# Performance work log

Hardware: AMD Instinct MI355X
Metric: run time of the kernel (lower is better)

## Reference

```python
import jax, jax.numpy as jnp
import numpy as np

N, M, E, D = 100000, 20000, 1600000, 128


def setup_inputs() -> dict:
    key = jax.random.key(0)
    ks = jax.random.split(key, 14)
    s = 1.0 / np.sqrt(D)
    inp = {
        "x": jax.random.normal(ks[0], (N, D), jnp.float32),
        "in_src": jax.random.randint(ks[1], (E,), 0, N),
        "in_dst": jax.random.randint(ks[2], (E,), 0, M),
        "has_src": jax.random.randint(ks[3], (E,), 0, M),
        "has_dst": jax.random.randint(ks[4], (E,), 0, N),
        "W1": jax.random.normal(ks[5], (D, D), jnp.float32) * s,
        "b1": jnp.zeros((D,), jnp.float32),
        "an1": jax.random.normal(ks[6], (D, 1), jnp.float32) * s,
        "ae1": jax.random.normal(ks[7], (D, 1), jnp.float32) * s,
        "W2": jax.random.normal(ks[8], (D, D), jnp.float32) * s,
        "b2": jnp.zeros((D,), jnp.float32),
        "an2": jax.random.normal(ks[9], (D, 1), jnp.float32) * s,
        "ae2": jax.random.normal(ks[10], (D, 1), jnp.float32) * s,
    }
    return inp


def _hgat_layer(x, W, b, an, ae, in_src, in_dst, has_src, has_dst, activate):
    h = x @ W + b                       # [N, D] fc transform
    n_attn = h @ an                     # [N, 1] node attn scores
    # node -> hyperedge ('in' edges). h_e is unset at this point (local_scope),
    # so the hyperedge bias term is zero; e = attn[src].
    e = n_attn[in_src]                  # [E, 1]
    # source uses F.softmax(e, dim=0): GLOBAL softmax over all edges
    attn = jax.nn.softmax(e, axis=0)    # [E, 1]
    h_e = jax.ops.segment_sum(attn * h[in_src], in_dst, num_segments=M)  # [M, D]
    e_attn = h_e @ ae                   # [M, 1] hyperedge attn scores
    # hyperedge -> node ('has' edges): bias is node attn score at dst
    e2 = e_attn[has_src] + n_attn[has_dst]  # [E, 1]
    attn2 = jax.nn.softmax(e2, axis=0)      # global softmax over all edges
    h_n = jax.ops.segment_sum(attn2 * h_e[has_src], has_dst, num_segments=N)  # [N, D]
    return jax.nn.relu(h_n) if activate else h_n


def reference(x, in_src, in_dst, has_src, has_dst,
              W1, b1, an1, ae1, W2, b2, an2, ae2):
    # layer 1 (activation=relu), layer 2 (no activation); dropout in eval mode
    h = _hgat_layer(x, W1, b1, an1, ae1, in_src, in_dst, has_src, has_dst, True)
    h = _hgat_layer(h, W2, b2, an2, ae2, in_src, in_dst, has_src, has_dst, False)
    return h
```

## Files before the change

kernel.cpp:

```cpp
#include <hip/hip_runtime.h>
#include <hip/hip_bf16.h>
#include <math.h>


typedef unsigned int u32;
typedef unsigned short u16;
typedef u16 u16x8 __attribute__((ext_vector_type(8)));
typedef short bf16x8 __attribute__((ext_vector_type(8)));
typedef float f32x4 __attribute__((ext_vector_type(4)));

#define NCONST 100000
#define MCONST 20000
#define ECONST 1600000
#define HCH2 32768
#define HBC 32
#define NCH_N 4

#define PBLK 256
#define PT 6250
#define SHB_IN 6
#define NBK_IN 313
#define SRCB_IN 17
#define SHB_HAS 8
#define NBK_HAS 391
#define SRCB_HAS 15

__device__ __forceinline__ u16 f2bf(float f) {
  u32 u = __float_as_uint(f);
  u += 0x7FFFu + ((u >> 16) & 1u);
  return (u16)(u >> 16);
}
__device__ __forceinline__ float bf2f(u16 b) {
  return __uint_as_float(((u32)b) << 16);
}

__global__ __launch_bounds__(256) void k_hpart2(const int* __restrict__ in_dst,
                                                const int* __restrict__ has_dst,
                                                int* __restrict__ partial) {
  __shared__ int hc[HCH2];
  int y = blockIdx.y;
  const int* __restrict__ arr = (y == 0) ? in_dst : has_dst;
  int lo = (y == 0) ? 0 : (y - 1) * HCH2;
  for (int i = threadIdx.x; i < HCH2; i += 256) hc[i] = 0;
  __syncthreads();
  int stride = gridDim.x * 256;
  int n4 = ECONST >> 2;
  const int4* a4 = (const int4*)arr;
  for (int i = blockIdx.x * 256 + threadIdx.x; i < n4; i += stride) {
    int4 v = a4[i];
    u32 a = (u32)(v.x - lo), b = (u32)(v.y - lo), c = (u32)(v.z - lo), d = (u32)(v.w - lo);
    if (a < HCH2) atomicAdd(&hc[a], 1);
    if (b < HCH2) atomicAdd(&hc[b], 1);
    if (c < HCH2) atomicAdd(&hc[c], 1);
    if (d < HCH2) atomicAdd(&hc[d], 1);
  }
  __syncthreads();
  int* out = partial + ((size_t)y * HBC + blockIdx.x) * HCH2;
  for (int i = threadIdx.x; i < HCH2; i += 256) out[i] = hc[i];
}

__global__ void k_scan1d(const int* __restrict__ partial, int nM, int nN,
                         int* __restrict__ off_in, int* __restrict__ off_has,
                         int* __restrict__ bsum) {
  __shared__ int sd[256];
  int y = blockIdx.y;
  int n = y ? nN : nM;
  int yoff = y;
  int* off = y ? off_has : off_in;
  int* bs = bsum + y * 128;
  int t = threadIdx.x;
  int base = blockIdx.x * 1024 + t * 4;
  int v[4];
#pragma unroll
  for (int k = 0; k < 4; ++k) {
    int j = base + k;
    int s = 0;
    if (j < n) {
      int chunk = j >> 15;
      int jl = j & (HCH2 - 1);
      const int* p = partial + ((size_t)(yoff + chunk) * HBC) * HCH2 + jl;
#pragma unroll
      for (int b = 0; b < HBC; ++b) s += p[(size_t)b * HCH2];
    }
    v[k] = s;
  }
  v[1] += v[0]; v[2] += v[1]; v[3] += v[2];
  int tot = v[3];
  sd[t] = tot;
  __syncthreads();
  for (int o = 1; o < 256; o <<= 1) {
    int x = (t >= o) ? sd[t - o] : 0;
    __syncthreads();
    sd[t] += x;
    __syncthreads();
  }
  int excl = sd[t] - tot;
#pragma unroll
  for (int k = 0; k < 4; ++k)
    if (base + k < n) off[base + k + 1] = v[k] + excl;
  if (t == 255) bs[blockIdx.x] = sd[255];
}

__global__ void k_scan2d(int* __restrict__ bsum, int nbM, int nbN) {
  __shared__ int sd[256];
  int* bs = bsum + blockIdx.x * 128;
  int nb = blockIdx.x ? nbN : nbM;
  int t = threadIdx.x;
  int v = (t < nb) ? bs[t] : 0;
  sd[t] = v;
  __syncthreads();
  for (int o = 1; o < 256; o <<= 1) {
    int x = (t >= o) ? sd[t - o] : 0;
    __syncthreads();
    sd[t] += x;
    __syncthreads();
  }
  if (t < nb) bs[t] = sd[t] - v;
}

__global__ void k_scan3d(int* __restrict__ off_in, int* __restrict__ off_has,
                         const int* __restrict__ bsum, int nM, int nN) {
  int y = blockIdx.y;
  int* off = y ? off_has : off_in;
  const int* bs = bsum + y * 128;
  int n = y ? nN : nM;
  int i = blockIdx.x * blockDim.x + threadIdx.x;
  int st = gridDim.x * blockDim.x;
  if (blockIdx.x == 0 && threadIdx.x == 0) off[0] = 0;
  for (; i < n; i += st) off[i + 1] += bs[i >> 10];
}

__global__ __launch_bounds__(256) void k_coarse(const int* __restrict__ in_dst,
                                                const int* __restrict__ has_dst,
                                                int* __restrict__ bb_in,
                                                int* __restrict__ bb_has) {
  __shared__ int h1[NBK_IN];
  __shared__ int h2[NBK_HAS];
  for (int i = threadIdx.x; i < NBK_IN; i += 256) h1[i] = 0;
  for (int i = threadIdx.x; i < NBK_HAS; i += 256) h2[i] = 0;
  __syncthreads();
  int c0 = blockIdx.x * PT, c1 = min(c0 + PT, ECONST);
  for (int i = c0 + threadIdx.x; i < c1; i += 256) {
    atomicAdd(&h1[in_dst[i] >> SHB_IN], 1);
    atomicAdd(&h2[has_dst[i] >> SHB_HAS], 1);
  }
  __syncthreads();
  int* o1 = bb_in + (size_t)blockIdx.x * NBK_IN;
  for (int i = threadIdx.x; i < NBK_IN; i += 256) o1[i] = h1[i];
  int* o2 = bb_has + (size_t)blockIdx.x * NBK_HAS;
  for (int i = threadIdx.x; i < NBK_HAS; i += 256) o2[i] = h2[i];
}

__global__ __launch_bounds__(256) void k_colscan(int* __restrict__ bb, int nbuk,
                                                 const int* __restrict__ off, int shb,
                                                 int segs) {
  __shared__ int sd[256];
  int b = blockIdx.x;
  int t = threadIdx.x;
  int v = bb[(size_t)t * nbuk + b];
  sd[t] = v;
  __syncthreads();
  for (int o = 1; o < 256; o <<= 1) {
    int x = (t >= o) ? sd[t - o] : 0;
    __syncthreads();
    sd[t] += x;
    __syncthreads();
  }
  bb[(size_t)t * nbuk + b] = sd[t] - v + off[min(b << shb, segs)];
}

template <int NBUK, int SHB, int SRCB>
__global__ __launch_bounds__(256) void k_stage(const int* __restrict__ dst,
                                               const int* __restrict__ srcv,
                                               const int* __restrict__ bb,
                                               int* __restrict__ ebuf) {
  __shared__ int hist[NBUK];
  __shared__ int loff[NBUK];
  __shared__ int gbase[NBUK];
  __shared__ int stage[PT];
  __shared__ int sd[256];
  int t = threadIdx.x;
  for (int i = t; i < NBUK; i += 256) hist[i] = 0;
  __syncthreads();
  int c0 = blockIdx.x * PT, c1 = min(c0 + PT, ECONST);
  for (int i = c0 + t; i < c1; i += 256) atomicAdd(&hist[dst[i] >> SHB], 1);
  __syncthreads();
  {
    int v0 = (2 * t < NBUK) ? hist[2 * t] : 0;
    int v1 = (2 * t + 1 < NBUK) ? hist[2 * t + 1] : 0;
    sd[t] = v0 + v1;
    __syncthreads();
    for (int o = 1; o < 256; o <<= 1) {
      int x = (t >= o) ? sd[t - o] : 0;
      __syncthreads();
      sd[t] += x;
      __syncthreads();
    }
    int excl = sd[t] - (v0 + v1);
    if (2 * t < NBUK) loff[2 * t] = excl;
    if (2 * t + 1 < NBUK) loff[2 * t + 1] = excl + v0;
  }
  __syncthreads();
  for (int i = t; i < NBUK; i += 256) {
    gbase[i] = bb[(size_t)blockIdx.x * NBUK + i];
    hist[i] = loff[i];
  }
  __syncthreads();
  for (int i = c0 + t; i < c1; i += 256) {
    int d = dst[i], s = srcv[i];
    int b = d >> SHB;
    int r = atomicAdd(&hist[b], 1);
    stage[r] = (b << 23) | ((d & ((1 << SHB) - 1)) << SRCB) | s;
  }
  __syncthreads();
  int tot = c1 - c0;
  for (int i = t; i < tot; i += 256) {
    int v = stage[i];
    int b = ((u32)v) >> 23;
    ebuf[gbase[b] + (i - loff[b])] = v & ((1 << 23) - 1);
  }
}

template <int SHB, int SRCB>
__global__ __launch_bounds__(256) void k_place(const int* __restrict__ off, int segs,
                                               const int* __restrict__ ebuf,
                                               int* __restrict__ csrc) {
  const int NSEG = 1 << SHB;
  __shared__ int cur[NSEG];
  int seg0 = blockIdx.x << SHB;
  if (seg0 >= segs) return;
  int segN = min(seg0 + NSEG, segs);
  for (int i = threadIdx.x; i < segN - seg0; i += 256) cur[i] = off[seg0 + i];
  __syncthreads();
  int start = off[seg0], end = off[segN];
  for (int i = start + threadIdx.x; i < end; i += 256) {
    int v = ebuf[i];
    int dloc = ((u32)v) >> SRCB;
    int pos = atomicAdd(&cur[dloc], 1);
    csrc[pos] = v & ((1 << SRCB) - 1);
  }
}

template <typename IT>
__global__ __launch_bounds__(256, 2) void k_fc(
    const IT* __restrict__ x, const float* __restrict__ W,
    const float* __restrict__ bias, const float* __restrict__ an,
    u16* __restrict__ h, float* __restrict__ na, int nrows) {
  __shared__ __align__(16) u16 sWT[128 * 136];
  int tid = threadIdx.x;
  int lane = tid & 63, w = tid >> 6;
  int cl = lane & 15, qg = lane >> 4;

  for (int i = tid * 4; i < 16384; i += 1024) {
    float4 v = *(const float4*)(W + i);
    int k = i >> 7, j = i & 127;
    sWT[(j + 0) * 136 + k] = f2bf(v.x);
    sWT[(j + 1) * 136 + k] = f2bf(v.y);
    sWT[(j + 2) * 136 + k] = f2bf(v.z);
    sWT[(j + 3) * 136 + k] = f2bf(v.w);
  }

  float anv[8], bv[8];
#pragma unroll
  for (int t = 0; t < 8; ++t) {
    anv[t] = an[t * 16 + cl];
    bv[t] = bias[t * 16 + cl];
  }

  int rbase = blockIdx.x * 128 + w * 32;
  bf16x8 afr[2][4];
#pragma unroll
  for (int g = 0; g < 2; ++g) {
    int r = rbase + g * 16 + cl;
    int rc = min(r, nrows - 1);
    const IT* xp = x + (size_t)rc * 128 + qg * 8;
#pragma unroll
    for (int s = 0; s < 4; ++s) {
      if constexpr (sizeof(IT) == 4) {
        float4 u0 = *(const float4*)(xp + s * 32);
        float4 u1 = *(const float4*)(xp + s * 32 + 4);
        bf16x8 a;
        a[0] = (short)f2bf(u0.x); a[1] = (short)f2bf(u0.y);
        a[2] = (short)f2bf(u0.z); a[3] = (short)f2bf(u0.w);
        a[4] = (short)f2bf(u1.x); a[5] = (short)f2bf(u1.y);
        a[6] = (short)f2bf(u1.z); a[7] = (short)f2bf(u1.w);
        afr[g][s] = a;
      } else {
        afr[g][s] = *(const bf16x8*)(xp + s * 32);
      }
    }
  }
  __syncthreads();

  f32x4 acc[2][8];
#pragma unroll
  for (int g = 0; g < 2; ++g)
#pragma unroll
    for (int t = 0; t < 8; ++t) {
      acc[g][t][0] = 0.f; acc[g][t][1] = 0.f; acc[g][t][2] = 0.f; acc[g][t][3] = 0.f;
    }

#pragma unroll
  for (int t = 0; t < 8; ++t) {
    bf16x8 bfrg[4];
    const u16* bp = sWT + (t * 16 + cl) * 136 + qg * 8;
#pragma unroll
    for (int s = 0; s < 4; ++s) bfrg[s] = *(const bf16x8*)(bp + s * 32);
#pragma unroll
    for (int s = 0; s < 4; ++s) {
#pragma unroll
      for (int g = 0; g < 2; ++g)
        acc[g][t] = __builtin_amdgcn_mfma_f32_16x16x32_bf16(afr[g][s], bfrg[s], acc[g][t],
                                                            0, 0, 0);
    }
  }

  float pa[2][4];
#pragma unroll
  for (int g = 0; g < 2; ++g)
#pragma unroll
    for (int reg = 0; reg < 4; ++reg) pa[g][reg] = 0.f;
#pragma unroll
  for (int g = 0; g < 2; ++g)
#pragma unroll
    for (int t = 0; t < 8; ++t)
#pragma unroll
      for (int reg = 0; reg < 4; ++reg)
        pa[g][reg] = fmaf(acc[g][t][reg] + bv[t], anv[t], pa[g][reg]);
#pragma unroll
  for (int g = 0; g < 2; ++g)
#pragma unroll
    for (int reg = 0; reg < 4; ++reg) {
      float v = pa[g][reg];
      v += __shfl_xor(v, 1, 64);
      v += __shfl_xor(v, 2, 64);
      v += __shfl_xor(v, 4, 64);
      v += __shfl_xor(v, 8, 64);
      pa[g][reg] = v;
    }
  if (cl == 0) {
#pragma unroll
    for (int g = 0; g < 2; ++g)
#pragma unroll
      for (int reg = 0; reg < 4; ++reg) {
        int r = rbase + g * 16 + qg * 4 + reg;
        if (r < nrows) na[r] = pa[g][reg];
      }
  }

  __syncthreads();
  u16* st = sWT + w * 32 * 136;
#pragma unroll
  for (int g = 0; g < 2; ++g)
#pragma unroll
    for (int t = 0; t < 8; ++t)
#pragma unroll
      for (int reg = 0; reg < 4; ++reg)
        st[(g * 16 + qg * 4 + reg) * 136 + t * 16 + cl] = f2bf(acc[g][t][reg] + bv[t]);
#pragma unroll
  for (int it = 0; it < 8; ++it) {
    int idx = it * 64 + lane;
    int row = idx >> 4, c = idx & 15;
    u16x8 v = *(const u16x8*)(st + row * 136 + c * 8);
    int r = rbase + row;
    if (r < nrows) *(u16x8*)(h + (size_t)r * 128 + c * 8) = v;
  }
}

__device__ __forceinline__ void merge_write(float m, float s, float2* __restrict__ pairs) {
  for (int o = 1; o < 64; o <<= 1) {
    float om = __shfl_xor(m, o, 64), os = __shfl_xor(s, o, 64);
    float nm = fmaxf(m, om);
    s = s * __expf(m - nm) + os * __expf(om - nm);
    m = nm;
  }
  __shared__ float sm[4], ss[4];
  int t = threadIdx.x;
  if ((t & 63) == 0) { sm[t >> 6] = m; ss[t >> 6] = s; }
  __syncthreads();
  if (t == 0) {
    for (int k = 1; k < 4; ++k) {
      float nm = fmaxf(m, sm[k]);
      s = s * __expf(m - nm) + ss[k] * __expf(sm[k] - nm);
      m = nm;
    }
    pairs[blockIdx.x] = make_float2(m, s);
  }
}

__global__ void k_sm1e(const float* __restrict__ na, const int* __restrict__ src, int n,
                       float2* __restrict__ pairs) {
  float m = -1e30f, s = 0.f;
  int i = blockIdx.x * blockDim.x + threadIdx.x;
  int st = gridDim.x * blockDim.x;
  for (; i < n; i += st) {
    float xv = na[src[i]];
    if (xv > m) { s *= __expf(m - xv); m = xv; }
    s += __expf(xv - m);
  }
  merge_write(m, s, pairs);
}

__global__ void k_sm2(const float* __restrict__ ea, const float* __restrict__ na,
                      const int* __restrict__ hs, const int* __restrict__ hd, int n,
                      float2* __restrict__ pairs) {
  float m = -1e30f, s = 0.f;
  int i = blockIdx.x * blockDim.x + threadIdx.x;
  int st = gridDim.x * blockDim.x;
  for (; i < n; i += st) {
    float xv = ea[hs[i]] + na[hd[i]];
    if (xv > m) { s *= __expf(m - xv); m = xv; }
    s += __expf(xv - m);
  }
  merge_write(m, s, pairs);
}

__global__ void k_smfin(const float2* __restrict__ pairs, int nb, float* __restrict__ out) {
  int t = threadIdx.x;
  float m = -1e30f, s = 0.f;
  for (int i = t; i < nb; i += 256) {
    float2 pr = pairs[i];
    float nm = fmaxf(m, pr.x);
    s = s * __expf(m - nm) + pr.y * __expf(pr.x - nm);
    m = nm;
  }
  for (int o = 1; o < 64; o <<= 1) {
    float om = __shfl_xor(m, o, 64), os = __shfl_xor(s, o, 64);
    float nm = fmaxf(m, om);
    s = s * __expf(m - nm) + os * __expf(om - nm);
    m = nm;
  }
  __shared__ float sm[4], ss[4];
  if ((t & 63) == 0) { sm[t >> 6] = m; ss[t >> 6] = s; }
  __syncthreads();
  if (t == 0) {
    for (int k = 1; k < 4; ++k) {
      float nm = fmaxf(m, sm[k]);
      s = s * __expf(m - nm) + ss[k] * __expf(sm[k] - nm);
      m = nm;
    }
    out[0] = m;
    out[1] = s;
  }
}

__global__ __launch_bounds__(256) void k_segA(
    const u16* __restrict__ h, const float* __restrict__ na,
    const float* __restrict__ scal, const int* __restrict__ csrc,
    const int* __restrict__ off, const float* __restrict__ ae, u16* __restrict__ he,
    float* __restrict__ ea, int m_count) {
  int wid = (blockIdx.x << 2) + (threadIdx.x >> 6);
  if (wid >= m_count) return;
  float mx = scal[0];
  float iz = 1.0f / scal[1];
  int lane = threadIdx.x & 63;
  int sub = lane >> 4, cl = lane & 15;
  int s = off[wid], t = off[wid + 1];
  float ax[8];
#pragma unroll
  for (int j = 0; j < 8; ++j) ax[j] = 0.f;
  for (int i = s + sub; i < t; i += 4) {
    int sr = csrc[i];
    float ww = __expf(na[sr] - mx) * iz;
    u16x8 v = *(const u16x8*)(h + (size_t)sr * 128 + cl * 8);
#pragma unroll
    for (int j = 0; j < 8; ++j) ax[j] = fmaf(ww, bf2f(v[j]), ax[j]);
  }
#pragma unroll
  for (int j = 0; j < 8; ++j) {
    ax[j] += __shfl_xor(ax[j], 16, 64);
    ax[j] += __shfl_xor(ax[j], 32, 64);
  }
  float4 a0 = *(const float4*)(ae + cl * 8);
  float4 a1 = *(const float4*)(ae + cl * 8 + 4);
  float pa = ax[0] * a0.x + ax[1] * a0.y + ax[2] * a0.z + ax[3] * a0.w +
             ax[4] * a1.x + ax[5] * a1.y + ax[6] * a1.z + ax[7] * a1.w;
  pa += __shfl_xor(pa, 1, 64);
  pa += __shfl_xor(pa, 2, 64);
  pa += __shfl_xor(pa, 4, 64);
  pa += __shfl_xor(pa, 8, 64);
  if (sub == 0) {
    u16x8 o;
#pragma unroll
    for (int j = 0; j < 8; ++j) o[j] = f2bf(ax[j]);
    *(u16x8*)(he + (size_t)wid * 128 + cl * 8) = o;
    if (cl == 0) ea[wid] = pa;
  }
}

template <int L1>
__global__ __launch_bounds__(256) void k_segB(
    const u16* __restrict__ he, const float* __restrict__ ea,
    const float* __restrict__ na, const float* __restrict__ scal,
    const int* __restrict__ csrc, const int* __restrict__ off,
    void* __restrict__ yout, int n_count) {
  int wid = (blockIdx.x << 2) + (threadIdx.x >> 6);
  if (wid >= n_count) return;
  float mx2 = scal[2];
  float iz2 = 1.0f / scal[3];
  int lane = threadIdx.x & 63;
  int sub = lane >> 4, cl = lane & 15;
  float nav = na[wid];
  int s = off[wid], t = off[wid + 1];
  float ax[8];
#pragma unroll
  for (int j = 0; j < 8; ++j) ax[j] = 0.f;
  for (int i = s + sub; i < t; i += 4) {
    int sr = csrc[i];
    float c = __expf(ea[sr] + nav - mx2) * iz2;
    u16x8 v = *(const u16x8*)(he + (size_t)sr * 128 + cl * 8);
#pragma unroll
    for (int j = 0; j < 8; ++j) ax[j] = fmaf(c, bf2f(v[j]), ax[j]);
  }
#pragma unroll
  for (int j = 0; j < 8; ++j) {
    ax[j] += __shfl_xor(ax[j], 16, 64);
    ax[j] += __shfl_xor(ax[j], 32, 64);
    if (L1) ax[j] = fmaxf(ax[j], 0.f);
  }
  if (sub == 0) {
    if (L1) {
      u16x8 o;
#pragma unroll
      for (int j = 0; j < 8; ++j) o[j] = f2bf(ax[j]);
      *(u16x8*)((u16*)yout + (size_t)wid * 128 + cl * 8) = o;
    } else {
      float4 A = make_float4(ax[0], ax[1], ax[2], ax[3]);
      float4 B = make_float4(ax[4], ax[5], ax[6], ax[7]);
      float* y = (float*)yout;
      *(float4*)(y + (size_t)wid * 128 + cl * 8) = A;
      *(float4*)(y + (size_t)wid * 128 + cl * 8 + 4) = B;
    }
  }
}

extern "C" void kernel_launch(void* const* d_in, const int* in_sizes, int n_in,
                              void* d_out, int out_size, void* d_ws, size_t ws_size,
                              hipStream_t stream) {
  const int N = NCONST, M = MCONST, E = ECONST;
  const float* x = (const float*)d_in[0];
  const int* in_src = (const int*)d_in[1];
  const int* in_dst = (const int*)d_in[2];
  const int* has_src = (const int*)d_in[3];
  const int* has_dst = (const int*)d_in[4];
  const float* W1 = (const float*)d_in[5];
  const float* b1 = (const float*)d_in[6];
  const float* an1 = (const float*)d_in[7];
  const float* ae1 = (const float*)d_in[8];
  const float* W2 = (const float*)d_in[9];
  const float* b2 = (const float*)d_in[10];
  const float* an2 = (const float*)d_in[11];
  const float* ae2 = (const float*)d_in[12];

  const size_t PARTIAL_BYTES = (size_t)(1 + NCH_N) * HBC * HCH2 * 4;

  char* p = (char*)d_ws;
  auto alloc = [&](size_t bytes) {
    char* q = p;
    p += (bytes + 255) & ~(size_t)255;
    return q;
  };
  u16* h = (u16*)alloc((size_t)N * 128 * 2);
  u16* he = (u16*)alloc((size_t)M * 128 * 2);
  float* na = (float*)alloc((size_t)N * 4);
  float* ea = (float*)alloc((size_t)M * 4);
  int* off_in = (int*)alloc((size_t)(M + 1) * 4);
  int* off_has = (int*)alloc((size_t)(N + 1) * 4);
  int* csrc_in = (int*)alloc((size_t)E * 4);
  int* csrc_has = (int*)alloc((size_t)E * 4);
  int* partial = (int*)alloc(PARTIAL_BYTES);
  int* ebuf = partial;
  int* bb_in = (int*)alloc((size_t)PBLK * NBK_IN * 4);
  int* bb_has = (int*)alloc((size_t)PBLK * NBK_HAS * 4);
  int* bsum = (int*)alloc(256 * 4);
  float2* pairs = (float2*)alloc(512 * 8);
  float* scal = (float*)alloc(64);
  if ((size_t)(p - (char*)d_ws) > ws_size) return;

  u16* y1b = (u16*)d_out;

  k_hpart2<<<dim3(HBC, 1 + NCH_N), 256, 0, stream>>>(in_dst, has_dst, partial);
  int nbM = (M + 1023) / 1024, nbN = (N + 1023) / 1024;
  k_scan1d<<<dim3(nbN, 2), 256, 0, stream>>>(partial, M, N, off_in, off_has, bsum);
  k_scan2d<<<2, 256, 0, stream>>>(bsum, nbM, nbN);
  k_scan3d<<<dim3(512, 2), 256, 0, stream>>>(off_in, off_has, bsum, M, N);

  k_coarse<<<PBLK, 256, 0, stream>>>(in_dst, has_dst, bb_in, bb_has);
  k_colscan<<<NBK_IN, 256, 0, stream>>>(bb_in, NBK_IN, off_in, SHB_IN, M);
  k_colscan<<<NBK_HAS, 256, 0, stream>>>(bb_has, NBK_HAS, off_has, SHB_HAS, N);
  k_stage<NBK_IN, SHB_IN, SRCB_IN><<<PBLK, 256, 0, stream>>>(in_dst, in_src, bb_in, ebuf);
  k_place<SHB_IN, SRCB_IN><<<NBK_IN, 256, 0, stream>>>(off_in, M, ebuf, csrc_in);
  k_stage<NBK_HAS, SHB_HAS, SRCB_HAS><<<PBLK, 256, 0, stream>>>(has_dst, has_src, bb_has,
                                                                ebuf);
  k_place<SHB_HAS, SRCB_HAS><<<NBK_HAS, 256, 0, stream>>>(off_has, N, ebuf, csrc_has);

  auto layer = [&](auto xin, const float* W, const float* b, const float* an_,
                   const float* ae_, auto seg_b) {
    using IT = typename std::remove_pointer<decltype(xin)>::type;
    k_fc<typename std::remove_const<IT>::type>
        <<<(N + 127) / 128, 256, 0, stream>>>(xin, W, b, an_, h, na, N);
    k_sm1e<<<512, 256, 0, stream>>>(na, in_src, E, pairs);
    k_smfin<<<1, 256, 0, stream>>>(pairs, 512, scal);
    k_segA<<<(M + 3) / 4, 256, 0, stream>>>(h, na, scal, csrc_in, off_in, ae_, he, ea, M);
    k_sm2<<<256, 256, 0, stream>>>(ea, na, has_src, has_dst, E, pairs);
    k_smfin<<<1, 256, 0, stream>>>(pairs, 256, scal + 2);
    seg_b();
  };

  layer((const float*)x, W1, b1, an1, ae1, [&] {
    k_segB<1><<<(N + 3) / 4, 256, 0, stream>>>(he, ea, na, scal, csrc_has, off_has,
                                               (void*)y1b, N);
  });
  layer((const u16*)y1b, W2, b2, an2, ae2, [&] {
    k_segB<0><<<(N + 3) / 4, 256, 0, stream>>>(he, ea, na, scal, csrc_has, off_has,
                                               d_out, N);
  });
}
```

Baseline: 481.5 us.

## Compute first softmax from source out-degrees in fc kernel; merge CSR build launches

Builds an out-degree histogram of in_src during preprocessing and uses it to compute the first global softmax's max/sum inside k_fc, where each node contributes its score weighted by its degree. This removes the per-layer gather over all E edges in k_sm1e. It also fuses the paired in/has colscan, stage and place launches into single 2D-grid kernels with separate ebuf regions, and raises k_fc occupancy hint to 3. The cost is extra histogram work for in_src and more shared memory and register pressure in k_fc.

Result: faster. 471.0 us (-2.2%).

```diff
diff --git a/kernel.cpp b/kernel.cpp
--- a/kernel.cpp
+++ b/kernel.cpp
@@ -1,6 +1,7 @@
 #include <hip/hip_runtime.h>
 #include <hip/hip_bf16.h>
 #include <math.h>
+#include <type_traits>
 
 
 typedef unsigned int u32;
@@ -36,11 +37,12 @@
 
 __global__ __launch_bounds__(256) void k_hpart2(const int* __restrict__ in_dst,
                                                 const int* __restrict__ has_dst,
+                                                const int* __restrict__ in_src,
                                                 int* __restrict__ partial) {
   __shared__ int hc[HCH2];
   int y = blockIdx.y;
-  const int* __restrict__ arr = (y == 0) ? in_dst : has_dst;
-  int lo = (y == 0) ? 0 : (y - 1) * HCH2;
+  const int* __restrict__ arr = (y == 0) ? in_dst : (y <= 4 ? has_dst : in_src);
+  int lo = (y == 0) ? 0 : (y <= 4 ? (y - 1) * HCH2 : (y - 5) * HCH2);
   for (int i = threadIdx.x; i < HCH2; i += 256) hc[i] = 0;
   __syncthreads();
   int stride = gridDim.x * 256;
@@ -61,13 +63,11 @@
 
 __global__ void k_scan1d(const int* __restrict__ partial, int nM, int nN,
                          int* __restrict__ off_in, int* __restrict__ off_has,
-                         int* __restrict__ bsum) {
+                         int* __restrict__ deg, int* __restrict__ bsum) {
   __shared__ int sd[256];
   int y = blockIdx.y;
   int n = y ? nN : nM;
-  int yoff = y;
-  int* off = y ? off_has : off_in;
-  int* bs = bsum + y * 128;
+  int rowbase = (y == 0) ? 0 : (y == 1 ? 1 : 5);
   int t = threadIdx.x;
   int base = blockIdx.x * 1024 + t * 4;
   int v[4];
@@ -78,12 +78,20 @@
     if (j < n) {
       int chunk = j >> 15;
       int jl = j & (HCH2 - 1);
-      const int* p = partial + ((size_t)(yoff + chunk) * HBC) * HCH2 + jl;
+      const int* p = partial + ((size_t)(rowbase + chunk) * HBC) * HCH2 + jl;
 #pragma unroll
       for (int b = 0; b < HBC; ++b) s += p[(size_t)b * HCH2];
     }
     v[k] = s;
   }
+  if (y == 2) {
+#pragma unroll
+    for (int k = 0; k < 4; ++k)
+      if (base + k < n) deg[base + k] = v[k];
+    return;
+  }
+  int* off = y ? off_has : off_in;
+  int* bs = bsum + y * 128;
   v[1] += v[0]; v[2] += v[1]; v[3] += v[2];
   int tot = v[3];
   sd[t] = tot;
@@ -151,13 +159,14 @@
   for (int i = threadIdx.x; i < NBK_HAS; i += 256) o2[i] = h2[i];
 }
 
-__global__ __launch_bounds__(256) void k_colscan(int* __restrict__ bb, int nbuk,
-                                                 const int* __restrict__ off, int shb,
-                                                 int segs) {
-  __shared__ int sd[256];
+template <int NBUK, int SHB>
+__device__ __forceinline__ void colscan_body(int* __restrict__ bb,
+                                             const int* __restrict__ off, int segs,
+                                             int* sd) {
   int b = blockIdx.x;
+  if (b >= NBUK) return;
   int t = threadIdx.x;
-  int v = bb[(size_t)t * nbuk + b];
+  int v = bb[(size_t)t * NBUK + b];
   sd[t] = v;
   __syncthreads();
   for (int o = 1; o < 256; o <<= 1) {
@@ -166,19 +175,26 @@
     sd[t] += x;
     __syncthreads();
   }
-  bb[(size_t)t * nbuk + b] = sd[t] - v + off[min(b << shb, segs)];
+  bb[(size_t)t * NBUK + b] = sd[t] - v + off[min(b << SHB, segs)];
+}
+
+__global__ __launch_bounds__(256) void k_colscan2(int* __restrict__ bb_in,
+                                                  const int* __restrict__ off_in,
+                                                  int* __restrict__ bb_has,
+                                                  const int* __restrict__ off_has) {
+  __shared__ int sd[256];
+  if (blockIdx.y == 0)
+    colscan_body<NBK_IN, SHB_IN>(bb_in, off_in, MCONST, sd);
+  else
+    colscan_body<NBK_HAS, SHB_HAS>(bb_has, off_has, NCONST, sd);
 }
 
 template <int NBUK, int SHB, int SRCB>
-__global__ __launch_bounds__(256) void k_stage(const int* __restrict__ dst,
-                                               const int* __restrict__ srcv,
-                                               const int* __restrict__ bb,
-                                               int* __restrict__ ebuf) {
-  __shared__ int hist[NBUK];
-  __shared__ int loff[NBUK];
-  __shared__ int gbase[NBUK];
-  __shared__ int stage[PT];
-  __shared__ int sd[256];
+__device__ __forceinline__ void stage_body(const int* __restrict__ dst,
+                                           const int* __restrict__ srcv,
+                                           const int* __restrict__ bb,
+                                           int* __restrict__ ebuf, int* hist, int* loff,
+                                           int* gbase, int* stg, int* sd) {
   int t = threadIdx.x;
   for (int i = t; i < NBUK; i += 256) hist[i] = 0;
   __syncthreads();
@@ -210,23 +226,40 @@
     int d = dst[i], s = srcv[i];
     int b = d >> SHB;
     int r = atomicAdd(&hist[b], 1);
-    stage[r] = (b << 23) | ((d & ((1 << SHB) - 1)) << SRCB) | s;
+    stg[r] = (b << 23) | ((d & ((1 << SHB) - 1)) << SRCB) | s;
   }
   __syncthreads();
   int tot = c1 - c0;
   for (int i = t; i < tot; i += 256) {
-    int v = stage[i];
+    int v = stg[i];
     int b = ((u32)v) >> 23;
     ebuf[gbase[b] + (i - loff[b])] = v & ((1 << 23) - 1);
   }
 }
 
+__global__ __launch_bounds__(256) void k_stage2(
+    const int* __restrict__ in_dst, const int* __restrict__ in_src,
+    const int* __restrict__ bb_in, int* __restrict__ ebuf_in,
+    const int* __restrict__ has_dst, const int* __restrict__ has_src,
+    const int* __restrict__ bb_has, int* __restrict__ ebuf_has) {
+  __shared__ int hist[NBK_HAS];
+  __shared__ int loff[NBK_HAS];
+  __shared__ int gbase[NBK_HAS];
+  __shared__ int stg[PT];
+  __shared__ int sd[256];
+  if (blockIdx.y == 0)
+    stage_body<NBK_IN, SHB_IN, SRCB_IN>(in_dst, in_src, bb_in, ebuf_in, hist, loff, gbase,
+                                        stg, sd);
+  else
+    stage_body<NBK_HAS, SHB_HAS, SRCB_HAS>(has_dst, has_src, bb_has, ebuf_has, hist, loff,
+                                           gbase, stg, sd);
+}
+
 template <int SHB, int SRCB>
-__global__ __launch_bounds__(256) void k_place(const int* __restrict__ off, int segs,
-                                               const int* __restrict__ ebuf,
-                                               int* __restrict__ csrc) {
+__device__ __forceinline__ void place_body(const int* __restrict__ off, int segs,
+                                           const int* __restrict__ ebuf,
+                                           int* __restrict__ csrc, int* cur) {
   const int NSEG = 1 << SHB;
-  __shared__ int cur[NSEG];
   int seg0 = blockIdx.x << SHB;
   if (seg0 >= segs) return;
   int segN = min(seg0 + NSEG, segs);
@@ -241,12 +274,46 @@
   }
 }
 
+__global__ __launch_bounds__(256) void k_place2(
+    const int* __restrict__ off_in, const int* __restrict__ ebuf_in,
+    int* __restrict__ csrc_in, const int* __restrict__ off_has,
+    const int* __restrict__ ebuf_has, int* __restrict__ csrc_has) {
+  __shared__ int cur[256];
+  if (blockIdx.y == 0)
+    place_body<SHB_IN, SRCB_IN>(off_in, MCONST, ebuf_in, csrc_in, cur);
+  else
+    place_body<SHB_HAS, SRCB_HAS>(off_has, NCONST, ebuf_has, csrc_has, cur);
+}
+
+__device__ __forceinline__ void merge_write(float m, float s, float2* __restrict__ pairs) {
+  for (int o = 1; o < 64; o <<= 1) {
+    float om = __shfl_xor(m, o, 64), os = __shfl_xor(s, o, 64);
+    float nm = fmaxf(m, om);
+    s = s * __expf(m - nm) + os * __expf(om - nm);
+    m = nm;
+  }
+  __shared__ float sm[4], ss[4];
+  int t = threadIdx.x;
+  if ((t & 63) == 0) { sm[t >> 6] = m; ss[t >> 6] = s; }
+  __syncthreads();
+  if (t == 0) {
+    for (int k = 1; k < 4; ++k) {
+      float nm = fmaxf(m, sm[k]);
+      s = s * __expf(m - nm) + ss[k] * __expf(sm[k] - nm);
+      m = nm;
+    }
+    pairs[blockIdx.x] = make_float2(m, s);
+  }
+}
+
 template <typename IT>
-__global__ __launch_bounds__(256, 2) void k_fc(
+__global__ __launch_bounds__(256, 3) void k_fc(
     const IT* __restrict__ x, const float* __restrict__ W,
     const float* __restrict__ bias, const float* __restrict__ an,
-    u16* __restrict__ h, float* __restrict__ na, int nrows) {
+    const int* __restrict__ deg, u16* __restrict__ h, float* __restrict__ na,
+    float2* __restrict__ pairs, int nrows) {
   __shared__ __align__(16) u16 sWT[128 * 136];
+  __shared__ float sNa[128];
   int tid = threadIdx.x;
   int lane = tid & 63, w = tid >> 6;
   int cl = lane & 15, qg = lane >> 4;
@@ -344,7 +411,11 @@
 #pragma unroll
       for (int reg = 0; reg < 4; ++reg) {
         int r = rbase + g * 16 + qg * 4 + reg;
-        if (r < nrows) na[r] = pa[g][reg];
+        int lidx = w * 32 + g * 16 + qg * 4 + reg;
+        if (r < nrows) {
+          na[r] = pa[g][reg];
+          sNa[lidx] = pa[g][reg];
+        }
       }
   }
 
@@ -365,40 +436,16 @@
     int r = rbase + row;
     if (r < nrows) *(u16x8*)(h + (size_t)r * 128 + c * 8) = v;
   }
-}
-
-__device__ __forceinline__ void merge_write(float m, float s, float2* __restrict__ pairs) {
-  for (int o = 1; o < 64; o <<= 1) {
-    float om = __shfl_xor(m, o, 64), os = __shfl_xor(s, o, 64);
-    float nm = fmaxf(m, om);
-    s = s * __expf(m - nm) + os * __expf(om - nm);
-    m = nm;
-  }
-  __shared__ float sm[4], ss[4];
-  int t = threadIdx.x;
-  if ((t & 63) == 0) { sm[t >> 6] = m; ss[t >> 6] = s; }
-  __syncthreads();
-  if (t == 0) {
-    for (int k = 1; k < 4; ++k) {
-      float nm = fmaxf(m, sm[k]);
-      s = s * __expf(m - nm) + ss[k] * __expf(sm[k] - nm);
-      m = nm;
-    }
-    pairs[blockIdx.x] = make_float2(m, s);
-  }
-}
-
-__global__ void k_sm1e(const float* __restrict__ na, const int* __restrict__ src, int n,
-                       float2* __restrict__ pairs) {
-  float m = -1e30f, s = 0.f;
-  int i = blockIdx.x * blockDim.x + threadIdx.x;
-  int st = gridDim.x * blockDim.x;
-  for (; i < n; i += st) {
-    float xv = na[src[i]];
-    if (xv > m) { s *= __expf(m - xv); m = xv; }
-    s += __expf(xv - m);
-  }
-  merge_write(m, s, pairs);
+
+  float m1 = -1e30f, s1 = 0.f;
+  if (tid < 128) {
+    int r = blockIdx.x * 128 + tid;
+    if (r < nrows) {
+      int d = deg[r];
+      if (d > 0) { m1 = sNa[tid]; s1 = (float)d; }
+    }
+  }
+  merge_write(m1, s1, pairs);
 }
 
 __global__ void k_sm2(const float* __restrict__ ea, const float* __restrict__ na,
@@ -552,7 +599,7 @@
   const float* an2 = (const float*)d_in[11];
   const float* ae2 = (const float*)d_in[12];
 
-  const size_t PARTIAL_BYTES = (size_t)(1 + NCH_N) * HBC * HCH2 * 4;
+  const size_t PARTIAL_BYTES = (size_t)9 * HBC * HCH2 * 4;
 
   char* p = (char*)d_ws;
   auto alloc = [&](size_t bytes) {
@@ -564,43 +611,43 @@
   u16* he = (u16*)alloc((size_t)M * 128 * 2);
   float* na = (float*)alloc((size_t)N * 4);
   float* ea = (float*)alloc((size_t)M * 4);
+  int* deg = (int*)alloc((size_t)N * 4);
   int* off_in = (int*)alloc((size_t)(M + 1) * 4);
   int* off_has = (int*)alloc((size_t)(N + 1) * 4);
   int* csrc_in = (int*)alloc((size_t)E * 4);
   int* csrc_has = (int*)alloc((size_t)E * 4);
   int* partial = (int*)alloc(PARTIAL_BYTES);
-  int* ebuf = partial;
+  int* ebuf_in = partial;
+  int* ebuf_has = partial + ECONST;
   int* bb_in = (int*)alloc((size_t)PBLK * NBK_IN * 4);
   int* bb_has = (int*)alloc((size_t)PBLK * NBK_HAS * 4);
   int* bsum = (int*)alloc(256 * 4);
-  float2* pairs = (float2*)alloc(512 * 8);
+  float2* pairs = (float2*)alloc(1024 * 8);
   float* scal = (float*)alloc(64);
   if ((size_t)(p - (char*)d_ws) > ws_size) return;
 
   u16* y1b = (u16*)d_out;
 
-  k_hpart2<<<dim3(HBC, 1 + NCH_N), 256, 0, stream>>>(in_dst, has_dst, partial);
+  k_hpart2<<<dim3(HBC, 9), 256, 0, stream>>>(in_dst, has_dst, in_src, partial);
   int nbM = (M + 1023) / 1024, nbN = (N + 1023) / 1024;
-  k_scan1d<<<dim3(nbN, 2), 256, 0, stream>>>(partial, M, N, off_in, off_has, bsum);
+  k_scan1d<<<dim3(nbN, 3), 256, 0, stream>>>(partial, M, N, off_in, off_has, deg, bsum);
   k_scan2d<<<2, 256, 0, stream>>>(bsum, nbM, nbN);
   k_scan3d<<<dim3(512, 2), 256, 0, stream>>>(off_in, off_has, bsum, M, N);
 
   k_coarse<<<PBLK, 256, 0, stream>>>(in_dst, has_dst, bb_in, bb_has);
-  k_colscan<<<NBK_IN, 256, 0, stream>>>(bb_in, NBK_IN, off_in, SHB_IN, M);
-  k_colscan<<<NBK_HAS, 256, 0, stream>>>(bb_has, NBK_HAS, off_has, SHB_HAS, N);
-  k_stage<NBK_IN, SHB_IN, SRCB_IN><<<PBLK, 256, 0, stream>>>(in_dst, in_src, bb_in, ebuf);
-  k_place<SHB_IN, SRCB_IN><<<NBK_IN, 256, 0, stream>>>(off_in, M, ebuf, csrc_in);
-  k_stage<NBK_HAS, SHB_HAS, SRCB_HAS><<<PBLK, 256, 0, stream>>>(has_dst, has_src, bb_has,
-                                                                ebuf);
-  k_place<SHB_HAS, SRCB_HAS><<<NBK_HAS, 256, 0, stream>>>(off_has, N, ebuf, csrc_has);
-
+  k_colscan2<<<dim3(NBK_HAS, 2), 256, 0, stream>>>(bb_in, off_in, bb_has, off_has);
+  k_stage2<<<dim3(PBLK, 2), 256, 0, stream>>>(in_dst, in_src, bb_in, ebuf_in, has_dst,
+                                              has_src, bb_has, ebuf_has);
+  k_place2<<<dim3(NBK_HAS, 2), 256, 0, stream>>>(off_in, ebuf_in, csrc_in, off_has,
+                                                 ebuf_has, csrc_has);
+
+  const int FCB = (N + 127) / 128;
   auto layer = [&](auto xin, const float* W, const float* b, const float* an_,
                    const float* ae_, auto seg_b) {
-    using IT = typename std::remove_pointer<decltype(xin)>::type;
-    k_fc<typename std::remove_const<IT>::type>
-        <<<(N + 127) / 128, 256, 0, stream>>>(xin, W, b, an_, h, na, N);
-    k_sm1e<<<512, 256, 0, stream>>>(na, in_src, E, pairs);
-    k_smfin<<<1, 256, 0, stream>>>(pairs, 512, scal);
+    using IT = typename std::remove_const<
+        typename std::remove_pointer<decltype(xin)>::type>::type;
+    k_fc<IT><<<FCB, 256, 0, stream>>>(xin, W, b, an_, deg, h, na, pairs, N);
+    k_smfin<<<1, 256, 0, stream>>>(pairs, FCB, scal);
     k_segA<<<(M + 3) / 4, 256, 0, stream>>>(h, na, scal, csrc_in, off_in, ae_, he, ea, M);
     k_sm2<<<256, 256, 0, stream>>>(ea, na, has_src, has_dst, E, pairs);
     k_smfin<<<1, 256, 0, stream>>>(pairs, 256, scal + 2);
```
